# Kernel tuning notes

Hardware: AMD Instinct MI355X
Metric: run time of the kernel (lower is better)

Reference implementation:

```python
import jax, jax.numpy as jnp
import numpy as np

HID = 512

def setup_inputs() -> dict:
    key = jax.random.key(0)
    k1, k2, k3, k4, k5, k6 = jax.random.split(key, 6)
    B, T, H = 32, 4096, HID
    enc_seq = jax.random.normal(k1, (B, T, H), dtype=jnp.float32)
    enc_mask = jax.random.randint(k2, (B, T), 0, 2, dtype=jnp.int32)
    dec_state = jax.random.normal(k3, (B, H), dtype=jnp.float32)
    # Linear weights, torch layout: y = x @ W.T
    scale = 1.0 / np.sqrt(H)
    W_h = jax.random.uniform(k4, (H, H), jnp.float32, -scale, scale)
    W_s = jax.random.uniform(k5, (H, H), jnp.float32, -scale, scale)
    v = jax.random.uniform(k6, (H,), jnp.float32, -scale, scale)
    return {"enc_seq": enc_seq, "enc_mask": enc_mask, "dec_state": dec_state,
            "W_h": W_h, "W_s": W_s, "v": v}

def reference(enc_seq, enc_mask, dec_state, W_h, W_s, v):
    # s: [B,H] -> [B,1,H] broadcast over T; h: [B,T,H]
    s = jnp.einsum('bh,kh->bk', dec_state, W_s)[:, None, :]
    h = jnp.einsum('bth,kh->btk', enc_seq, W_h)
    e = jnp.einsum('bth,h->bt', jnp.tanh(h + s), v)  # [B,T]
    e = jnp.where(enc_mask == 0, jnp.float32(-1e9), e)
    a = jax.nn.softmax(e, axis=1)  # [B,T]
    ctx = jnp.einsum('bt,bth->bh', a, enc_seq)  # [B,H]
    return (ctx, a)
```

## Files before the change

kernel.cpp:

```cpp
#include <hip/hip_runtime.h>
#include <hip/hip_bf16.h>
#include <cstdint>
#include <cstddef>

#define HID 512
#define T_SZ 4096

typedef __bf16 bf16x8 __attribute__((ext_vector_type(8)));
typedef float f32x4 __attribute__((ext_vector_type(4)));

__device__ __forceinline__ unsigned short f2bf_rne(float f) {
    unsigned int u = __float_as_uint(f);
    unsigned int r = (u + 0x7FFFu + ((u >> 16) & 1u)) >> 16;
    return (unsigned short)r;
}

__device__ __forceinline__ bf16x8 pack8(float4 x0, float4 x1) {
    bf16x8 r;
    r[0] = (__bf16)x0.x; r[1] = (__bf16)x0.y; r[2] = (__bf16)x0.z; r[3] = (__bf16)x0.w;
    r[4] = (__bf16)x1.x; r[5] = (__bf16)x1.y; r[6] = (__bf16)x1.z; r[7] = (__bf16)x1.w;
    return r;
}

__device__ __forceinline__ float fast_tanh(float x) {
    float e = __expf(2.0f * x);
    return 1.0f - 2.0f / (e + 1.0f);
}

__global__ void k_s(const float* __restrict__ dec, const float* __restrict__ Ws,
                    float* __restrict__ s) {
    int idx = blockIdx.x * 256 + threadIdx.x;
    int b = idx >> 9, n = idx & 511;
    const float4* dp = reinterpret_cast<const float4*>(dec + (size_t)b * HID);
    const float4* wp = reinterpret_cast<const float4*>(Ws + (size_t)n * HID);
    float acc = 0.f;
#pragma unroll 8
    for (int i = 0; i < HID / 4; ++i) {
        float4 d = dp[i], w = wp[i];
        acc += d.x * w.x + d.y * w.y + d.z * w.z + d.w * w.w;
    }
    s[idx] = acc;
}

__global__ void k_pack(const float* __restrict__ Wh, uint4* __restrict__ Wb) {
    int idx = blockIdx.x * 256 + threadIdx.x;
    int n = idx >> 6;
    int k0 = (idx & 63) * 8;
    const float4* p = reinterpret_cast<const float4*>(Wh + (size_t)n * HID + k0);
    float4 x0 = p[0], x1 = p[1];
    uint4 w;
    w.x = f2bf_rne(x0.x) | ((unsigned)f2bf_rne(x0.y) << 16);
    w.y = f2bf_rne(x0.z) | ((unsigned)f2bf_rne(x0.w) << 16);
    w.z = f2bf_rne(x1.x) | ((unsigned)f2bf_rne(x1.y) << 16);
    w.w = f2bf_rne(x1.z) | ((unsigned)f2bf_rne(x1.w) << 16);
    int n4 = n >> 4, c = n & 15, kk = k0 >> 5, g = (k0 >> 3) & 3;
    Wb[(size_t)kk * 2048 + n4 * 64 + g * 16 + c] = w;
}

__global__ void __launch_bounds__(256, 2) k_gemm_e(
    const float* __restrict__ enc, const uint4* __restrict__ Wb,
    const float* __restrict__ s, const float* __restrict__ v,
    float* __restrict__ part_e) {
    __shared__ __align__(16) unsigned char As[65536];
    __shared__ float red[4][64];

    const int tid = threadIdx.x;
    const int p = blockIdx.x;
    const int logical = (p & 7) * 512 + (p >> 3);
    const int h = logical & 1;
    const int m = logical >> 1;
    const size_t row0 = (size_t)m * 64;
    const int b = (int)(row0 >> 12);

    const int lane = tid & 63, wid = tid >> 6;
    const int c = lane & 15, g4 = lane >> 4;

    {
        const float* base = enc + row0 * HID;
#pragma unroll
        for (int i = 0; i < 16; ++i) {
            int f = i * 256 + tid;
            float4 x0 = *reinterpret_cast<const float4*>(base + (size_t)f * 8);
            float4 x1 = *reinterpret_cast<const float4*>(base + (size_t)f * 8 + 4);
            int row = f >> 6, c8 = f & 63;
            int kk = c8 >> 2, g = c8 & 3;
            int chunk = (row >> 4) * 64 + g * 16 + (row & 15);
            int byte = (kk * 4096 + chunk * 16) ^ (((((kk & 3) << 1) | (g & 1))) << 4);
            *reinterpret_cast<bf16x8*>(&As[byte]) = pack8(x0, x1);
        }
    }

    float sv_s[4], sv_v[4];
#pragma unroll
    for (int ni = 0; ni < 4; ++ni) {
        int n = (h * 16 + wid * 4 + ni) * 16 + c;
        sv_s[ni] = s[b * HID + n];
        sv_v[ni] = v[n];
    }
    __syncthreads();

    const uint4* Bg = Wb + (h * 16 + wid * 4) * 64 + lane;

    uint4 bR[3][4];
#pragma unroll
    for (int d = 0; d < 3; ++d)
#pragma unroll
        for (int ni = 0; ni < 4; ++ni)
            bR[d][ni] = Bg[(size_t)d * 2048 + ni * 64];

    bf16x8 af[2][4];
#pragma unroll
    for (int mi = 0; mi < 4; ++mi) {
        int byte = ((mi * 64 + lane) * 16) ^ ((((0 & 3) << 1) | ((lane >> 4) & 1)) << 4);
        af[0][mi] = *reinterpret_cast<const bf16x8*>(&As[byte]);
    }

    f32x4 acc[4][4] = {};

#pragma unroll
    for (int kk = 0; kk < 16; ++kk) {
        if (kk < 15) {
#pragma unroll
            for (int mi = 0; mi < 4; ++mi) {
                int byte = ((kk + 1) * 4096 + (mi * 64 + lane) * 16)
                         ^ (((((kk + 1) & 3) << 1) | ((lane >> 4) & 1)) << 4);
                af[(kk + 1) & 1][mi] = *reinterpret_cast<const bf16x8*>(&As[byte]);
            }
        }
#pragma unroll
        for (int mi = 0; mi < 4; ++mi)
#pragma unroll
            for (int ni = 0; ni < 4; ++ni)
                acc[mi][ni] = __builtin_amdgcn_mfma_f32_16x16x32_bf16(
                    af[kk & 1][mi], *reinterpret_cast<bf16x8*>(&bR[kk % 3][ni]),
                    acc[mi][ni], 0, 0, 0);
        if (kk + 3 <= 15) {
#pragma unroll
            for (int ni = 0; ni < 4; ++ni)
                bR[kk % 3][ni] = Bg[(size_t)(kk + 3) * 2048 + ni * 64];
        }
    }

    float e_part[4][4] = {};
#pragma unroll
    for (int ni = 0; ni < 4; ++ni) {
        float sn = sv_s[ni], vn = sv_v[ni];
#pragma unroll
        for (int mi = 0; mi < 4; ++mi)
#pragma unroll
            for (int r = 0; r < 4; ++r)
                e_part[mi][r] += fast_tanh(acc[mi][ni][r] + sn) * vn;
    }
#pragma unroll
    for (int mm = 1; mm <= 8; mm <<= 1)
#pragma unroll
        for (int mi = 0; mi < 4; ++mi)
#pragma unroll
            for (int r = 0; r < 4; ++r)
                e_part[mi][r] += __shfl_xor(e_part[mi][r], mm);

    if (c == 0) {
#pragma unroll
        for (int mi = 0; mi < 4; ++mi)
#pragma unroll
            for (int r = 0; r < 4; ++r)
                red[wid][mi * 16 + g4 * 4 + r] = e_part[mi][r];
    }
    __syncthreads();
    if (tid < 64)
        part_e[(size_t)h * 131072 + row0 + tid] =
            red[0][tid] + red[1][tid] + red[2][tid] + red[3][tid];
}

__global__ void k_softmax(const float* __restrict__ part_e, float* __restrict__ a,
                          const int* __restrict__ mask) {
    int b = blockIdx.x, tid = threadIdx.x;
    int lane = tid & 63, wid = tid >> 6;
    __shared__ float red[16];
    float vals[4]; int ms[4];
    float mx = -1e30f;
#pragma unroll
    for (int j = 0; j < 4; ++j) {
        size_t t = (size_t)b * T_SZ + tid + j * 1024;
        vals[j] = part_e[t] + part_e[131072 + t];
        ms[j] = mask[t];
        if (ms[j]) mx = fmaxf(mx, vals[j]);
    }
#pragma unroll
    for (int m = 32; m >= 1; m >>= 1) mx = fmaxf(mx, __shfl_xor(mx, m));
    if (lane == 0) red[wid] = mx;
    __syncthreads();
    if (tid == 0) {
        float m2 = red[0];
        for (int i = 1; i < 16; ++i) m2 = fmaxf(m2, red[i]);
        red[0] = m2;
    }
    __syncthreads();
    mx = red[0];
    __syncthreads();
    float pv[4]; float sum = 0.f;
#pragma unroll
    for (int j = 0; j < 4; ++j) { pv[j] = ms[j] ? __expf(vals[j] - mx) : 0.f; sum += pv[j]; }
#pragma unroll
    for (int m = 32; m >= 1; m >>= 1) sum += __shfl_xor(sum, m);
    if (lane == 0) red[wid] = sum;
    __syncthreads();
    if (tid == 0) {
        float s2 = 0.f;
        for (int i = 0; i < 16; ++i) s2 += red[i];
        red[0] = s2;
    }
    __syncthreads();
    float inv = 1.f / red[0];
#pragma unroll
    for (int j = 0; j < 4; ++j)
        a[(size_t)b * T_SZ + tid + j * 1024] = pv[j] * inv;
}

__global__ void k_ctx(const float* __restrict__ enc, const float* __restrict__ a,
                      float2* __restrict__ part) {
    int ts = blockIdx.x, b = blockIdx.y, tid = threadIdx.x;
    size_t rbase = (size_t)b * T_SZ + (size_t)ts * 128;
    const float2* ep = reinterpret_cast<const float2*>(enc + rbase * HID) + tid;
    const float* ap = a + rbase;
    float ax = 0.f, ay = 0.f, bx = 0.f, by = 0.f;
#pragma unroll 2
    for (int t = 0; t < 128; t += 2) {
        float a0 = ap[t], a1 = ap[t + 1];
        float2 e0 = ep[(size_t)t * 256], e1 = ep[(size_t)(t + 1) * 256];
        ax += a0 * e0.x; ay += a0 * e0.y;
        bx += a1 * e1.x; by += a1 * e1.y;
    }
    float2 r; r.x = ax + bx; r.y = ay + by;
    part[(size_t)(b * 32 + ts) * 256 + tid] = r;
}

__global__ void k_ctxred(const float* __restrict__ part, float* __restrict__ ctx) {
    int idx = blockIdx.x * 256 + threadIdx.x;
    int b = idx >> 9, h = idx & 511;
    float sum = 0.f;
#pragma unroll
    for (int ts = 0; ts < 32; ++ts) sum += part[(size_t)(b * 32 + ts) * 512 + h];
    ctx[idx] = sum;
}

extern "C" void kernel_launch(void* const* d_in, const int* in_sizes, int n_in,
                              void* d_out, int out_size, void* d_ws, size_t ws_size,
                              hipStream_t stream) {
    const float* enc  = (const float*)d_in[0];
    const int*   mask = (const int*)d_in[1];
    const float* dec  = (const float*)d_in[2];
    const float* Wh   = (const float*)d_in[3];
    const float* Ws   = (const float*)d_in[4];
    const float* v    = (const float*)d_in[5];

    float* out = (float*)d_out;
    float* ctx = out;
    float* a   = out + 16384;

    float* ws     = (float*)d_ws;
    float* s      = ws;
    uint4* Wb     = (uint4*)(ws + 16384);
    float* part_e = ws + 16384 + 131072;
    float* part   = part_e + 262144;

    hipLaunchKernelGGL(k_s,      dim3(64),      dim3(256),  0, stream, dec, Ws, s);
    hipLaunchKernelGGL(k_pack,   dim3(128),     dim3(256),  0, stream, Wh, Wb);
    hipLaunchKernelGGL(k_gemm_e, dim3(4096),    dim3(256),  0, stream, enc, Wb, s, v, part_e);
    hipLaunchKernelGGL(k_softmax,dim3(32),      dim3(1024), 0, stream, part_e, a, mask);
    hipLaunchKernelGGL(k_ctx,    dim3(32, 32),  dim3(256),  0, stream, enc, a, (float2*)part);
    hipLaunchKernelGGL(k_ctxred, dim3(64),      dim3(256),  0, stream, part, ctx);
}
```

Baseline: 178.6 us.

## Split GEMM tile across 8 waves and drop LDS swizzle in k_gemm_e

Doubles the k_gemm_e block to 512 threads arranged as a 2x4 wave grid, so each wave computes a 32x64 sub-tile instead of 64x64. The enc staging loop now writes LDS in fragment order without the XOR swizzle, and B-fragment prefetch depth drops from 3 to 2. The launch bound is raised to (512, 4). The goal is more waves to hide MFMA and memory latency. In exchange, each wave reloads the W fragments for fewer rows. Global loads of enc become row-strided across lanes, and the tighter register budget implied by the new launch bounds may cause spills.

```diff
diff --git a/kernel.cpp b/kernel.cpp
--- a/kernel.cpp
+++ b/kernel.cpp
@@ -57,12 +57,12 @@
     Wb[(size_t)kk * 2048 + n4 * 64 + g * 16 + c] = w;
 }
 
-__global__ void __launch_bounds__(256, 2) k_gemm_e(
+__global__ void __launch_bounds__(512, 4) k_gemm_e(
     const float* __restrict__ enc, const uint4* __restrict__ Wb,
     const float* __restrict__ s, const float* __restrict__ v,
     float* __restrict__ part_e) {
     __shared__ __align__(16) unsigned char As[65536];
-    __shared__ float red[4][64];
+    __shared__ float red[2][4][32];
 
     const int tid = threadIdx.x;
     const int p = blockIdx.x;
@@ -74,79 +74,75 @@
 
     const int lane = tid & 63, wid = tid >> 6;
     const int c = lane & 15, g4 = lane >> 4;
+    const int wm = wid >> 2, wn = wid & 3;
+
+    float sv_s[4], sv_v[4];
+#pragma unroll
+    for (int ni = 0; ni < 4; ++ni) {
+        int n = (h * 16 + wn * 4 + ni) * 16 + c;
+        sv_s[ni] = s[b * HID + n];
+        sv_v[ni] = v[n];
+    }
 
     {
         const float* base = enc + row0 * HID;
 #pragma unroll
-        for (int i = 0; i < 16; ++i) {
-            int f = i * 256 + tid;
-            float4 x0 = *reinterpret_cast<const float4*>(base + (size_t)f * 8);
-            float4 x1 = *reinterpret_cast<const float4*>(base + (size_t)f * 8 + 4);
-            int row = f >> 6, c8 = f & 63;
-            int kk = c8 >> 2, g = c8 & 3;
-            int chunk = (row >> 4) * 64 + g * 16 + (row & 15);
-            int byte = (kk * 4096 + chunk * 16) ^ (((((kk & 3) << 1) | (g & 1))) << 4);
-            *reinterpret_cast<bf16x8*>(&As[byte]) = pack8(x0, x1);
+        for (int i = 0; i < 8; ++i) {
+            int G = i * 512 + tid;
+            int kk = G >> 8, cin = G & 255;
+            int mi = cin >> 6, gg = (cin >> 4) & 3, cc = cin & 15;
+            const float* src = base + (size_t)(mi * 16 + cc) * HID + kk * 32 + gg * 8;
+            float4 x0 = *reinterpret_cast<const float4*>(src);
+            float4 x1 = *reinterpret_cast<const float4*>(src + 4);
+            *reinterpret_cast<bf16x8*>(&As[G * 16]) = pack8(x0, x1);
         }
     }
-
-    float sv_s[4], sv_v[4];
-#pragma unroll
-    for (int ni = 0; ni < 4; ++ni) {
-        int n = (h * 16 + wid * 4 + ni) * 16 + c;
-        sv_s[ni] = s[b * HID + n];
-        sv_v[ni] = v[n];
-    }
-    __syncthreads();
-
-    const uint4* Bg = Wb + (h * 16 + wid * 4) * 64 + lane;
-
-    uint4 bR[3][4];
-#pragma unroll
-    for (int d = 0; d < 3; ++d)
+    __syncthreads();
+
+    const uint4* Bg = Wb + (size_t)(h * 16 + wn * 4) * 64 + lane;
+
+    uint4 bR[2][4];
+#pragma unroll
+    for (int d = 0; d < 2; ++d)
 #pragma unroll
         for (int ni = 0; ni < 4; ++ni)
             bR[d][ni] = Bg[(size_t)d * 2048 + ni * 64];
 
-    bf16x8 af[2][4];
-#pragma unroll
-    for (int mi = 0; mi < 4; ++mi) {
-        int byte = ((mi * 64 + lane) * 16) ^ ((((0 & 3) << 1) | ((lane >> 4) & 1)) << 4);
-        af[0][mi] = *reinterpret_cast<const bf16x8*>(&As[byte]);
-    }
-
-    f32x4 acc[4][4] = {};
+    bf16x8 af[2][2];
+#pragma unroll
+    for (int mi = 0; mi < 2; ++mi)
+        af[0][mi] = *reinterpret_cast<const bf16x8*>(&As[((wm * 2 + mi) * 64 + lane) * 16]);
+
+    f32x4 acc[2][4] = {};
 
 #pragma unroll
     for (int kk = 0; kk < 16; ++kk) {
         if (kk < 15) {
 #pragma unroll
-            for (int mi = 0; mi < 4; ++mi) {
-                int byte = ((kk + 1) * 4096 + (mi * 64 + lane) * 16)
-                         ^ (((((kk + 1) & 3) << 1) | ((lane >> 4) & 1)) << 4);
-                af[(kk + 1) & 1][mi] = *reinterpret_cast<const bf16x8*>(&As[byte]);
-            }
+            for (int mi = 0; mi < 2; ++mi)
+                af[(kk + 1) & 1][mi] = *reinterpret_cast<const bf16x8*>(
+                    &As[(kk + 1) * 4096 + ((wm * 2 + mi) * 64 + lane) * 16]);
         }
 #pragma unroll
-        for (int mi = 0; mi < 4; ++mi)
+        for (int mi = 0; mi < 2; ++mi)
 #pragma unroll
             for (int ni = 0; ni < 4; ++ni)
                 acc[mi][ni] = __builtin_amdgcn_mfma_f32_16x16x32_bf16(
-                    af[kk & 1][mi], *reinterpret_cast<bf16x8*>(&bR[kk % 3][ni]),
+                    af[kk & 1][mi], *reinterpret_cast<bf16x8*>(&bR[kk & 1][ni]),
                     acc[mi][ni], 0, 0, 0);
-        if (kk + 3 <= 15) {
+        if (kk + 2 <= 15) {
 #pragma unroll
             for (int ni = 0; ni < 4; ++ni)
-                bR[kk % 3][ni] = Bg[(size_t)(kk + 3) * 2048 + ni * 64];
+                bR[kk & 1][ni] = Bg[(size_t)(kk + 2) * 2048 + ni * 64];
         }
     }
 
-    float e_part[4][4] = {};
+    float e_part[2][4] = {};
 #pragma unroll
     for (int ni = 0; ni < 4; ++ni) {
         float sn = sv_s[ni], vn = sv_v[ni];
 #pragma unroll
-        for (int mi = 0; mi < 4; ++mi)
+        for (int mi = 0; mi < 2; ++mi)
 #pragma unroll
             for (int r = 0; r < 4; ++r)
                 e_part[mi][r] += fast_tanh(acc[mi][ni][r] + sn) * vn;
@@ -154,22 +150,24 @@
 #pragma unroll
     for (int mm = 1; mm <= 8; mm <<= 1)
 #pragma unroll
-        for (int mi = 0; mi < 4; ++mi)
+        for (int mi = 0; mi < 2; ++mi)
 #pragma unroll
             for (int r = 0; r < 4; ++r)
                 e_part[mi][r] += __shfl_xor(e_part[mi][r], mm);
 
     if (c == 0) {
 #pragma unroll
-        for (int mi = 0; mi < 4; ++mi)
+        for (int mi = 0; mi < 2; ++mi)
 #pragma unroll
             for (int r = 0; r < 4; ++r)
-                red[wid][mi * 16 + g4 * 4 + r] = e_part[mi][r];
-    }
-    __syncthreads();
-    if (tid < 64)
+                red[wm][wn][mi * 16 + g4 * 4 + r] = e_part[mi][r];
+    }
+    __syncthreads();
+    if (tid < 64) {
+        int wm2 = tid >> 5, rl = tid & 31;
         part_e[(size_t)h * 131072 + row0 + tid] =
-            red[0][tid] + red[1][tid] + red[2][tid] + red[3][tid];
+            red[wm2][0][rl] + red[wm2][1][rl] + red[wm2][2][rl] + red[wm2][3][rl];
+    }
 }
 
 __global__ void k_softmax(const float* __restrict__ part_e, float* __restrict__ a,
@@ -266,7 +264,7 @@
 
     hipLaunchKernelGGL(k_s,      dim3(64),      dim3(256),  0, stream, dec, Ws, s);
     hipLaunchKernelGGL(k_pack,   dim3(128),     dim3(256),  0, stream, Wh, Wb);
-    hipLaunchKernelGGL(k_gemm_e, dim3(4096),    dim3(256),  0, stream, enc, Wb, s, v, part_e);
+    hipLaunchKernelGGL(k_gemm_e, dim3(4096),    dim3(512),  0, stream, enc, Wb, s, v, part_e);
     hipLaunchKernelGGL(k_softmax,dim3(32),      dim3(1024), 0, stream, part_e, a, mask);
     hipLaunchKernelGGL(k_ctx,    dim3(32, 32),  dim3(256),  0, stream, enc, a, (float2*)part);
     hipLaunchKernelGGL(k_ctxred, dim3(64),      dim3(256),  0, stream, part, ctx);
```

New measurement: 214.1 us. 1.2x slower.

## Restructure GEMM: stage W_h in LDS, stream enc directly from global into registers

Applied to the files above, without the earlier changes.

The fused GEMM+tanh kernel now uses 512-thread blocks, each covering 256 rows and a 128-column strip of W_h, split into four column strips. The whole strip of packed bf16 weights is loaded into LDS with global_load_lds, and enc rows are read straight from global into registers with a 3-deep prefetch, then converted to bf16 per k-step. This removes the enc-to-LDS staging pass, but each enc row is now read by four blocks instead of two. It also uses 128KB of LDS at one block per CU, and softmax must sum four partial-score buffers.

```diff
diff --git a/kernel.cpp b/kernel.cpp
--- a/kernel.cpp
+++ b/kernel.cpp
@@ -25,6 +25,12 @@
 __device__ __forceinline__ float fast_tanh(float x) {
     float e = __expf(2.0f * x);
     return 1.0f - 2.0f / (e + 1.0f);
+}
+
+__device__ __forceinline__ void gload_lds16(const void* g, void* l) {
+    __builtin_amdgcn_global_load_lds(
+        (const __attribute__((address_space(1))) unsigned int*)g,
+        (__attribute__((address_space(3))) unsigned int*)l, 16, 0, 0);
 }
 
 __global__ void k_s(const float* __restrict__ dec, const float* __restrict__ Ws,
@@ -57,88 +63,84 @@
     Wb[(size_t)kk * 2048 + n4 * 64 + g * 16 + c] = w;
 }
 
-__global__ void __launch_bounds__(256, 2) k_gemm_e(
+__global__ void __launch_bounds__(512, 1) k_gemm_e(
     const float* __restrict__ enc, const uint4* __restrict__ Wb,
     const float* __restrict__ s, const float* __restrict__ v,
     float* __restrict__ part_e) {
-    __shared__ __align__(16) unsigned char As[65536];
-    __shared__ float red[4][64];
+    __shared__ __align__(16) unsigned char Bs[131072];
+    __shared__ float red[2][256];
 
     const int tid = threadIdx.x;
     const int p = blockIdx.x;
-    const int logical = (p & 7) * 512 + (p >> 3);
-    const int h = logical & 1;
-    const int m = logical >> 1;
-    const size_t row0 = (size_t)m * 64;
+    const int logical = (p & 7) * 256 + (p >> 3);
+    const int strip = logical & 3;
+    const int mt = logical >> 2;
+    const size_t row0 = (size_t)mt * 256;
     const int b = (int)(row0 >> 12);
 
     const int lane = tid & 63, wid = tid >> 6;
-    const int c = lane & 15, g4 = lane >> 4;
-
-    {
-        const float* base = enc + row0 * HID;
-#pragma unroll
-        for (int i = 0; i < 16; ++i) {
-            int f = i * 256 + tid;
-            float4 x0 = *reinterpret_cast<const float4*>(base + (size_t)f * 8);
-            float4 x1 = *reinterpret_cast<const float4*>(base + (size_t)f * 8 + 4);
-            int row = f >> 6, c8 = f & 63;
-            int kk = c8 >> 2, g = c8 & 3;
-            int chunk = (row >> 4) * 64 + g * 16 + (row & 15);
-            int byte = (kk * 4096 + chunk * 16) ^ (((((kk & 3) << 1) | (g & 1))) << 4);
-            *reinterpret_cast<bf16x8*>(&As[byte]) = pack8(x0, x1);
-        }
-    }
+    const int c16 = lane & 15, g4 = lane >> 4;
+    const int wm = wid >> 1, wn = wid & 1;
 
     float sv_s[4], sv_v[4];
 #pragma unroll
     for (int ni = 0; ni < 4; ++ni) {
-        int n = (h * 16 + wid * 4 + ni) * 16 + c;
+        int n = strip * 128 + wn * 64 + ni * 16 + c16;
         sv_s[ni] = s[b * HID + n];
         sv_v[ni] = v[n];
     }
-    __syncthreads();
-
-    const uint4* Bg = Wb + (h * 16 + wid * 4) * 64 + lane;
-
-    uint4 bR[3][4];
-#pragma unroll
-    for (int d = 0; d < 3; ++d)
-#pragma unroll
-        for (int ni = 0; ni < 4; ++ni)
-            bR[d][ni] = Bg[(size_t)d * 2048 + ni * 64];
-
-    bf16x8 af[2][4];
+
+    const float* Asrc[4];
+#pragma unroll
+    for (int mi = 0; mi < 4; ++mi)
+        Asrc[mi] = enc + (row0 + wm * 64 + mi * 16 + c16) * HID + g4 * 8;
+
+    float4 arlo[3][4], arhi[3][4];
+
 #pragma unroll
     for (int mi = 0; mi < 4; ++mi) {
-        int byte = ((mi * 64 + lane) * 16) ^ ((((0 & 3) << 1) | ((lane >> 4) & 1)) << 4);
-        af[0][mi] = *reinterpret_cast<const bf16x8*>(&As[byte]);
-    }
+        arlo[0][mi] = *reinterpret_cast<const float4*>(Asrc[mi]);
+        arhi[0][mi] = *reinterpret_cast<const float4*>(Asrc[mi] + 4);
+        arlo[1][mi] = *reinterpret_cast<const float4*>(Asrc[mi] + 32);
+        arhi[1][mi] = *reinterpret_cast<const float4*>(Asrc[mi] + 36);
+    }
+
+#pragma unroll
+    for (int r = 0; r < 16; ++r) {
+        int j = r * 8 + wid, kk = j >> 3, n4q = j & 7;
+        gload_lds16(Wb + (size_t)kk * 2048 + (strip * 8 + n4q) * 64 + lane,
+                    &Bs[(size_t)(r * 512 + wid * 64) * 16]);
+    }
+    __syncthreads();
 
     f32x4 acc[4][4] = {};
 
 #pragma unroll
     for (int kk = 0; kk < 16; ++kk) {
-        if (kk < 15) {
+        if (kk + 2 <= 15) {
 #pragma unroll
             for (int mi = 0; mi < 4; ++mi) {
-                int byte = ((kk + 1) * 4096 + (mi * 64 + lane) * 16)
-                         ^ (((((kk + 1) & 3) << 1) | ((lane >> 4) & 1)) << 4);
-                af[(kk + 1) & 1][mi] = *reinterpret_cast<const bf16x8*>(&As[byte]);
+                arlo[(kk + 2) % 3][mi] =
+                    *reinterpret_cast<const float4*>(Asrc[mi] + (kk + 2) * 32);
+                arhi[(kk + 2) % 3][mi] =
+                    *reinterpret_cast<const float4*>(Asrc[mi] + (kk + 2) * 32 + 4);
             }
         }
+        bf16x8 af[4];
+#pragma unroll
+        for (int mi = 0; mi < 4; ++mi)
+            af[mi] = pack8(arlo[kk % 3][mi], arhi[kk % 3][mi]);
+        bf16x8 bfr[4];
+#pragma unroll
+        for (int ni = 0; ni < 4; ++ni)
+            bfr[ni] = *reinterpret_cast<const bf16x8*>(
+                &Bs[(size_t)((kk * 8 + wn * 4 + ni) * 64 + lane) * 16]);
 #pragma unroll
         for (int mi = 0; mi < 4; ++mi)
 #pragma unroll
             for (int ni = 0; ni < 4; ++ni)
                 acc[mi][ni] = __builtin_amdgcn_mfma_f32_16x16x32_bf16(
-                    af[kk & 1][mi], *reinterpret_cast<bf16x8*>(&bR[kk % 3][ni]),
-                    acc[mi][ni], 0, 0, 0);
-        if (kk + 3 <= 15) {
-#pragma unroll
-            for (int ni = 0; ni < 4; ++ni)
-                bR[kk % 3][ni] = Bg[(size_t)(kk + 3) * 2048 + ni * 64];
-        }
+                    af[mi], bfr[ni], acc[mi][ni], 0, 0, 0);
     }
 
     float e_part[4][4] = {};
@@ -159,17 +161,16 @@
             for (int r = 0; r < 4; ++r)
                 e_part[mi][r] += __shfl_xor(e_part[mi][r], mm);
 
-    if (c == 0) {
+    if (c16 == 0) {
 #pragma unroll
         for (int mi = 0; mi < 4; ++mi)
 #pragma unroll
             for (int r = 0; r < 4; ++r)
-                red[wid][mi * 16 + g4 * 4 + r] = e_part[mi][r];
-    }
-    __syncthreads();
-    if (tid < 64)
-        part_e[(size_t)h * 131072 + row0 + tid] =
-            red[0][tid] + red[1][tid] + red[2][tid] + red[3][tid];
+                red[wn][wm * 64 + mi * 16 + g4 * 4 + r] = e_part[mi][r];
+    }
+    __syncthreads();
+    if (tid < 256)
+        part_e[(size_t)strip * 131072 + row0 + tid] = red[0][tid] + red[1][tid];
 }
 
 __global__ void k_softmax(const float* __restrict__ part_e, float* __restrict__ a,
@@ -182,7 +183,7 @@
 #pragma unroll
     for (int j = 0; j < 4; ++j) {
         size_t t = (size_t)b * T_SZ + tid + j * 1024;
-        vals[j] = part_e[t] + part_e[131072 + t];
+        vals[j] = part_e[t] + part_e[131072 + t] + part_e[262144 + t] + part_e[393216 + t];
         ms[j] = mask[t];
         if (ms[j]) mx = fmaxf(mx, vals[j]);
     }
@@ -262,11 +263,11 @@
     float* s      = ws;
     uint4* Wb     = (uint4*)(ws + 16384);
     float* part_e = ws + 16384 + 131072;
-    float* part   = part_e + 262144;
+    float* part   = part_e + 524288;
 
     hipLaunchKernelGGL(k_s,      dim3(64),      dim3(256),  0, stream, dec, Ws, s);
     hipLaunchKernelGGL(k_pack,   dim3(128),     dim3(256),  0, stream, Wh, Wb);
-    hipLaunchKernelGGL(k_gemm_e, dim3(4096),    dim3(256),  0, stream, enc, Wb, s, v, part_e);
+    hipLaunchKernelGGL(k_gemm_e, dim3(2048),    dim3(512),  0, stream, enc, Wb, s, v, part_e);
     hipLaunchKernelGGL(k_softmax,dim3(32),      dim3(1024), 0, stream, part_e, a, mask);
     hipLaunchKernelGGL(k_ctx,    dim3(32, 32),  dim3(256),  0, stream, enc, a, (float2*)part);
     hipLaunchKernelGGL(k_ctxred, dim3(64),      dim3(256),  0, stream, part, ctx);
```

Result: slower. 368.6 us (+106.4%).
